# Kernel optimization log

Measured on AMD Instinct MI355X. Metric: run time of the kernel, lower is better.

The kernel has to match this reference:

```python
import jax, jax.numpy as jnp
import numpy as np

B, N, DIM = 1, 32768, 512
H, DH = 8, 64            # heads, dim_head
INNER = H * DH           # 512
L = 64                   # n_cluster = clip(N // (16*16) + 1, 16, 64) = 64 landmarks
ITERS = 6                # pinv_iterations
KS = 33                  # residual_conv_kernel


def setup_inputs() -> dict:
    key = jax.random.key(0)
    k1, k2, k3, k4, k5 = jax.random.split(key, 5)
    x = jax.random.normal(k1, (B, N, DIM), jnp.float32)
    labels = jax.random.randint(k2, (N,), 0, L, jnp.int32)  # kmeans cluster ids (no_grad constants)
    Wqkv = jax.random.normal(k3, (DIM, 3 * INNER), jnp.float32) * 0.02
    Wout = jax.random.normal(k4, (INNER, DIM), jnp.float32) * 0.02
    bout = jnp.zeros((DIM,), jnp.float32)
    res_kernel = jax.random.normal(k5, (H, 1, KS, 1), jnp.float32) * 0.05  # depthwise conv, groups=H
    return dict(x=x, Wqkv=Wqkv, Wout=Wout, bout=bout, res_kernel=res_kernel, labels=labels)


def _pinv(a, iters=ITERS):
    # Moore-Penrose via Newton-Schulz, matching moore_penrose_iter_pinv (global max normalization)
    abs_a = jnp.abs(a)
    z = a.swapaxes(-1, -2) / (abs_a.sum(-1).max() * abs_a.sum(-2).max())
    I = jnp.eye(a.shape[-1], dtype=a.dtype)
    for _ in range(iters):
        az = a @ z
        z = 0.25 * z @ (13.0 * I - az @ (15.0 * I - az @ (7.0 * I - az)))
    return z


def _pool_mean(t, seg):
    # ragged per-cluster mean: t [b,h,n,d], seg [n] sorted cluster ids -> [b,h,L,d]
    b, h, n, d = t.shape
    flat = t.transpose(2, 0, 1, 3).reshape(n, b * h * d)
    sums = jax.ops.segment_sum(flat, seg, num_segments=L)
    counts = jax.ops.segment_sum(jnp.ones((n,), t.dtype), seg, num_segments=L)
    means = sums / jnp.maximum(counts, 1.0)[:, None]
    return means.reshape(L, b, h, d).transpose(1, 2, 0, 3)


def reference(x, Wqkv, Wout, bout, res_kernel, labels):
    # cluster sort / unsort (mirrors x[:, index] ... out[:, index_ori])
    index = jnp.argsort(labels)
    index_ori = jnp.argsort(index)
    seg = labels[index]                      # sorted segment ids
    xp = x[:, index]

    qkv = xp @ Wqkv                          # [b,n,3*inner]
    q, k, v = jnp.split(qkv, 3, axis=-1)
    to_bhnd = lambda t: t.reshape(B, N, H, DH).transpose(0, 2, 1, 3)
    q, k, v = to_bhnd(q), to_bhnd(k), to_bhnd(v)

    ql = _pool_mean(q, seg)                  # [b,h,L,d]
    kl = _pool_mean(k, seg)

    # note: original forward never multiplies by self.scale
    attn1 = jax.nn.softmax(jnp.einsum('bhnd,bhld->bhnl', q, kl), axis=-1)   # [b,h,n,L]
    attn2 = jax.nn.softmax(jnp.einsum('bhid,bhjd->bhij', ql, kl), axis=-1)  # [b,h,L,L]
    attn3 = jax.nn.softmax(jnp.einsum('bhld,bhnd->bhln', ql, k), axis=-1)   # [b,h,L,n]

    out = attn1 @ (_pinv(attn2) @ (attn3 @ v))                              # [b,h,n,d]

    # residual depthwise conv over token axis (Conv2d(h,h,(33,1),groups=h))
    res = jax.lax.conv_general_dilated(
        v, res_kernel, window_strides=(1, 1),
        padding=((KS // 2, KS // 2), (0, 0)),
        dimension_numbers=('NCHW', 'OIHW', 'NCHW'),
        feature_group_count=H)
    out = out + res

    out = out.transpose(0, 2, 1, 3).reshape(B, N, INNER)
    out = out @ Wout + bout
    return out[:, index_ori]
```

## Files before the change

kernel.cpp:

```cpp
#include <hip/hip_runtime.h>
#include <hip/hip_bf16.h>

#define N_TOK 32768
#define DIMC  512
#define NH    8
#define DHD   64
#define NL    64
#define KSZ   33
#define QKVC  1536
#define NCHUNK 64

typedef _Float16 f16;
typedef _Float16 f16x8 __attribute__((ext_vector_type(8)));
typedef _Float16 f16x4 __attribute__((ext_vector_type(4)));
typedef float    f32x4 __attribute__((ext_vector_type(4)));

#define GLOAD_LDS16(gp, lp) \
    __builtin_amdgcn_global_load_lds((const __attribute__((address_space(1))) void*)(gp), \
                                     (__attribute__((address_space(3))) void*)(lp), 16, 0, 0)

__global__ void transpose_k(const float* __restrict__ W, f16* __restrict__ WT, int R, int C) {
    __shared__ float tile[32][33];
    int bx = blockIdx.x * 32, by = blockIdx.y * 32;
    int tx = threadIdx.x, ty = threadIdx.y;
    #pragma unroll
    for (int i = 0; i < 32; i += 8)
        tile[ty + i][tx] = W[(size_t)(by + ty + i) * C + bx + tx];
    __syncthreads();
    #pragma unroll
    for (int i = 0; i < 32; i += 8)
        WT[(size_t)(bx + ty + i) * R + by + tx] = (f16)tile[tx][ty + i];
}

__global__ void hist_k(const int* __restrict__ labels, int* __restrict__ counts) {
    __shared__ int hloc[NL];
    int t = threadIdx.x;
    if (t < NL) hloc[t] = 0;
    __syncthreads();
    int i = blockIdx.x * 256 + t;
    atomicAdd(&hloc[labels[i]], 1);
    __syncthreads();
    if (t < NL) atomicAdd(&counts[t], hloc[t]);
}

__global__ void scan_k(const int* __restrict__ counts, int* __restrict__ base) {
    if (threadIdx.x == 0) {
        int s = 0;
        for (int l = 0; l < NL; ++l) { base[l] = s; s += counts[l]; }
    }
}

__global__ __launch_bounds__(256) void compact_k(const int* __restrict__ labels,
                                                 const int* __restrict__ base,
                                                 int* __restrict__ indexArr) {
    const int l = blockIdx.x;
    __shared__ int wtot[4];
    __shared__ int s_run;
    int t = threadIdx.x, lane = t & 63, w = t >> 6;
    if (t == 0) s_run = base[l];
    __syncthreads();
    for (int c0 = 0; c0 < N_TOK; c0 += 256) {
        int ii = c0 + t;
        bool flag = (labels[ii] == l);
        unsigned long long mask = __ballot(flag);
        int before = __popcll(mask & ((1ull << lane) - 1ull));
        if (lane == 0) wtot[w] = __popcll(mask);
        __syncthreads();
        int off = 0;
        #pragma unroll
        for (int ww = 0; ww < 4; ++ww) off += (ww < w) ? wtot[ww] : 0;
        int tot = wtot[0] + wtot[1] + wtot[2] + wtot[3];
        int rb = s_run;
        if (flag) indexArr[rb + off + before] = ii;
        __syncthreads();
        if (t == 0) s_run = rb + tot;
    }
}

__global__ __launch_bounds__(256) void gather_cvt_k(const float4* __restrict__ x4,
                                                    const int* __restrict__ indexArr,
                                                    f16x4* __restrict__ xh4) {
    int t = threadIdx.x;
    int row = blockIdx.x * 2 + (t >> 7);
    int c4 = t & 127;
    int j = indexArr[row];
    float4 v = x4[(size_t)j * 128 + c4];
    f16x4 o = { (f16)v.x, (f16)v.y, (f16)v.z, (f16)v.w };
    xh4[(size_t)row * 128 + c4] = o;
}

template<int BNTOT, bool OUT_F32, int NY>
__global__ __launch_bounds__(512, 4) void gemm_k512(const f16* __restrict__ A, const f16* __restrict__ BT,
                                                    void* __restrict__ Cout, const float* __restrict__ bias,
                                                    const int* __restrict__ scatterIdx) {
    constexpr int K = 512;
    constexpr int NKT = K / 32;
    __shared__ f16 As[3][128 * 32];
    __shared__ f16 Bs[3][256 * 32];
    const int t = threadIdx.x;
    const int orig = blockIdx.x + gridDim.x * blockIdx.y;
    constexpr int NWG = 256 * NY;
    constexpr int CPX = NWG / 8;
    const int lin = (orig & 7) * CPX + (orig >> 3);
    const int mBase = (lin / NY) * 128;
    const int nBase = (lin % NY) * 256;
    const int w = t >> 6, lane = t & 63;
    const int wm = w >> 2, wn = w & 3;
    const int lr = lane & 15, lk = lane >> 4;
    const int kc = (lk ^ ((lr >> 1) & 3)) * 8;
    f32x4 acc[4][4];
    #pragma unroll
    for (int m = 0; m < 4; ++m)
        #pragma unroll
        for (int n = 0; n < 4; ++n) acc[m][n] = (f32x4){0.f, 0.f, 0.f, 0.f};

    auto stage = [&](int buf, int kt) {
        {
            int id = t;
            int row = id >> 2, c = id & 3;
            int cg = c ^ ((row >> 1) & 3);
            GLOAD_LDS16(&A[(size_t)(mBase + row) * K + kt * 32 + cg * 8],
                        &As[buf][(size_t)(w * 64) * 8]);
        }
        #pragma unroll
        for (int r = 0; r < 2; ++r) {
            int id = r * 512 + t;
            int row = id >> 2, c = id & 3;
            int cg = c ^ ((row >> 1) & 3);
            GLOAD_LDS16(&BT[(size_t)(nBase + row) * K + kt * 32 + cg * 8],
                        &Bs[buf][(size_t)(r * 512 + w * 64) * 8]);
        }
    };
    auto compute = [&](int buf) {
        f16x8 af[4], bf[4];
        #pragma unroll
        for (int m = 0; m < 4; ++m)
            af[m] = *(const f16x8*)&As[buf][(wm * 64 + m * 16 + lr) * 32 + kc];
        #pragma unroll
        for (int n = 0; n < 4; ++n)
            bf[n] = *(const f16x8*)&Bs[buf][(wn * 64 + n * 16 + lr) * 32 + kc];
        #pragma unroll
        for (int m = 0; m < 4; ++m)
            #pragma unroll
            for (int n = 0; n < 4; ++n)
                acc[m][n] = __builtin_amdgcn_mfma_f32_16x16x32_f16(bf[n], af[m], acc[m][n], 0, 0, 0);
    };

    stage(0, 0);
    asm volatile("" ::: "memory");
    stage(1, 1);
    for (int kt = 0; kt < NKT; ++kt) {
        if (kt < NKT - 1) {
            asm volatile("s_waitcnt vmcnt(3)" ::: "memory");
        } else {
            asm volatile("s_waitcnt vmcnt(0)" ::: "memory");
        }
        __builtin_amdgcn_s_barrier();
        if (kt + 2 < NKT) stage((kt + 2) % 3, kt + 2);
        compute(kt % 3);
    }

    #pragma unroll
    for (int m = 0; m < 4; ++m) {
        int row = mBase + wm * 64 + m * 16 + lr;
        int srow = OUT_F32 ? scatterIdx[row] : row;
        #pragma unroll
        for (int n = 0; n < 4; ++n) {
            int col = nBase + wn * 64 + n * 16 + lk * 4;
            if constexpr (OUT_F32) {
                float4 bv = *(const float4*)&bias[col];
                float4 sv = make_float4(acc[m][n][0] + bv.x, acc[m][n][1] + bv.y,
                                        acc[m][n][2] + bv.z, acc[m][n][3] + bv.w);
                *(float4*)&((float*)Cout)[(size_t)srow * BNTOT + col] = sv;
            } else {
                f16x4 hv = { (f16)acc[m][n][0], (f16)acc[m][n][1],
                             (f16)acc[m][n][2], (f16)acc[m][n][3] };
                *(f16x4*)&((f16*)Cout)[(size_t)srow * BNTOT + col] = hv;
            }
        }
    }
}

__global__ __launch_bounds__(256) void pool_part_k(const f16* __restrict__ qkvh,
                                                   const int* __restrict__ base,
                                                   const int* __restrict__ counts,
                                                   float* __restrict__ psum) {
    int l = blockIdx.x, g = blockIdx.y;
    int t = threadIdx.x;
    int c = t & 127, rg = t >> 7;
    int b0 = base[l], cnt = counts[l];
    f32x4 a0 = {0.f,0.f,0.f,0.f}, a1 = {0.f,0.f,0.f,0.f};
    for (int p = g * 2 + rg; p < cnt; p += 8) {
        f16x8 v = *(const f16x8*)&qkvh[(size_t)(b0 + p) * QKVC + c * 8];
        a0[0] += (float)v[0]; a0[1] += (float)v[1]; a0[2] += (float)v[2]; a0[3] += (float)v[3];
        a1[0] += (float)v[4]; a1[1] += (float)v[5]; a1[2] += (float)v[6]; a1[3] += (float)v[7];
    }
    __shared__ f32x4 red[2][128][2];
    red[rg][c][0] = a0; red[rg][c][1] = a1;
    __syncthreads();
    if (t < 128) {
        f32x4 s0 = red[0][t][0] + red[1][t][0];
        f32x4 s1 = red[0][t][1] + red[1][t][1];
        size_t o = ((size_t)g * NL + l) * 1024 + t * 8;
        *(f32x4*)&psum[o] = s0;
        *(f32x4*)&psum[o + 4] = s1;
    }
}

__global__ __launch_bounds__(256) void pool_fin_k(const float* __restrict__ psum,
                                                  const int* __restrict__ counts,
                                                  float* __restrict__ ql, float* __restrict__ kl,
                                                  f16* __restrict__ qlh, f16* __restrict__ klh) {
    int l = blockIdx.x;
    int t = threadIdx.x;
    int bse = t * 4;
    float inv = 1.0f / (float)(counts[l] > 0 ? counts[l] : 1);
    f32x4 s = {0.f,0.f,0.f,0.f};
    #pragma unroll
    for (int g = 0; g < 4; ++g)
        s += *(const f32x4*)&psum[((size_t)g * NL + l) * 1024 + bse];
    s *= inv;
    f16x4 hv = { (f16)s[0], (f16)s[1], (f16)s[2], (f16)s[3] };
    if (bse < 512) {
        int h = bse >> 6, d0 = bse & 63;
        size_t o = ((size_t)(h * 64 + l)) * 64 + d0;
        *(f32x4*)&ql[o] = s;
        *(f16x4*)&qlh[o] = hv;
    } else {
        int bb = bse - 512;
        int h = bb >> 6, d0 = bb & 63;
        size_t o = ((size_t)(h * 64 + l)) * 64 + d0;
        *(f32x4*)&kl[o] = s;
        *(f16x4*)&klh[o] = hv;
    }
}

__global__ __launch_bounds__(256) void attn2_k(const float* __restrict__ ql, const float* __restrict__ kl,
                                               float* __restrict__ a_out, float* __restrict__ mrow,
                                               float* __restrict__ mcol) {
    int h = blockIdx.x;
    __shared__ float qs[64][65], ks[64][65], a[64][65];
    __shared__ float red[64][4];
    __shared__ float rowv[64], colv[64];
    int t = threadIdx.x;
    for (int idx = t; idx < 4096; idx += 256) {
        int r = idx >> 6, c = idx & 63;
        qs[r][c] = ql[h * 4096 + idx];
        ks[r][c] = kl[h * 4096 + idx];
    }
    __syncthreads();
    int i = t >> 2, q4 = t & 3, j0 = q4 * 16;
    float o[16];
    #pragma unroll
    for (int jj = 0; jj < 16; ++jj) o[jj] = 0.f;
    for (int d = 0; d < 64; ++d) {
        float qv = qs[i][d];
        #pragma unroll
        for (int jj = 0; jj < 16; ++jj) o[jj] += qv * ks[j0 + jj][d];
    }
    float pmx = o[0];
    #pragma unroll
    for (int jj = 1; jj < 16; ++jj) pmx = fmaxf(pmx, o[jj]);
    red[i][q4] = pmx;
    __syncthreads();
    float rm = fmaxf(fmaxf(red[i][0], red[i][1]), fmaxf(red[i][2], red[i][3]));
    float psum = 0.f;
    #pragma unroll
    for (int jj = 0; jj < 16; ++jj) { o[jj] = expf(o[jj] - rm); psum += o[jj]; }
    __syncthreads();
    red[i][q4] = psum;
    __syncthreads();
    float rs = red[i][0] + red[i][1] + red[i][2] + red[i][3];
    float inv = 1.0f / rs;
    #pragma unroll
    for (int jj = 0; jj < 16; ++jj) { o[jj] *= inv; a[i][j0 + jj] = o[jj]; }
    __syncthreads();
    for (int idx = t; idx < 4096; idx += 256) a_out[h * 4096 + idx] = a[idx >> 6][idx & 63];
    float rsum = 0.f;
    #pragma unroll
    for (int jj = 0; jj < 16; ++jj) rsum += o[jj];
    __syncthreads();
    red[i][q4] = rsum;
    __syncthreads();
    if (q4 == 0) rowv[i] = red[i][0] + red[i][1] + red[i][2] + red[i][3];
    float csum = 0.f;
    #pragma unroll
    for (int jj = 0; jj < 16; ++jj) csum += a[j0 + jj][i];
    __syncthreads();
    red[i][q4] = csum;
    __syncthreads();
    if (q4 == 0) colv[i] = red[i][0] + red[i][1] + red[i][2] + red[i][3];
    __syncthreads();
    if (t == 0) {
        float mr = rowv[0], mc = colv[0];
        for (int j = 1; j < 64; ++j) { mr = fmaxf(mr, rowv[j]); mc = fmaxf(mc, colv[j]); }
        mrow[h] = mr; mcol[h] = mc;
    }
}

__global__ __launch_bounds__(256) void pinv_zmatT_k(const float* __restrict__ a_g,
                                                    const float* __restrict__ mrow,
                                                    const float* __restrict__ mcol,
                                                    const float* __restrict__ T,
                                                    f16* __restrict__ MthHi, f16* __restrict__ MthLo) {
    const int h = blockIdx.x;
    __shared__ float zf[64][68];
    __shared__ float Cf[64][68];
    __shared__ f16 aRh[64][72], aRl[64][72];
    __shared__ f16 zFh[64][72], zFl[64][72];
    __shared__ f16 cRh[64][72], cRl[64][72];
    __shared__ f16 ceCh[64][72], ceCl[64][72];
    __shared__ f16 dCh[64][72], dCl[64][72];
    const int t = threadIdx.x;
    const int w = t >> 6, lane = t & 63;
    const int lr = lane & 15, lk = lane >> 4;
    float mr = mrow[0], mc = mcol[0];
    #pragma unroll
    for (int k = 1; k < 8; ++k) { mr = fmaxf(mr, mrow[k]); mc = fmaxf(mc, mcol[k]); }
    const float inv0 = 1.0f / (mr * mc);
    for (int idx = t; idx < 4096; idx += 256) {
        int r = idx >> 6, c = idx & 63;
        float av = a_g[h * 4096 + idx];
        f16 hv = (f16)av;
        aRh[r][c] = hv; aRl[r][c] = (f16)(av - (float)hv);
        zf[c][r] = av * inv0;
    }
    __syncthreads();

    f32x4 po[4];
    auto product = [&](const f16 (*Xh)[72], const f16 (*Xl)[72],
                       const f16 (*Yh)[72], const f16 (*Yl)[72]) {
        #pragma unroll
        for (int n = 0; n < 4; ++n) po[n] = (f32x4){0.f, 0.f, 0.f, 0.f};
        #pragma unroll
        for (int ck = 0; ck < 2; ++ck) {
            f16x8 axh = *(const f16x8*)&Xh[w * 16 + lr][ck * 32 + lk * 8];
            f16x8 axl = *(const f16x8*)&Xl[w * 16 + lr][ck * 32 + lk * 8];
            #pragma unroll
            for (int n = 0; n < 4; ++n) {
                f16x8 byh = *(const f16x8*)&Yh[n * 16 + lr][ck * 32 + lk * 8];
                f16x8 byl = *(const f16x8*)&Yl[n * 16 + lr][ck * 32 + lk * 8];
                po[n] = __builtin_amdgcn_mfma_f32_16x16x32_f16(byh, axh, po[n], 0, 0, 0);
                po[n] = __builtin_amdgcn_mfma_f32_16x16x32_f16(byl, axh, po[n], 0, 0, 0);
                po[n] = __builtin_amdgcn_mfma_f32_16x16x32_f16(byh, axl, po[n], 0, 0, 0);
            }
        }
    };

    for (int it = 0; it < 6; ++it) {
        for (int idx = t; idx < 4096; idx += 256) {
            int r = idx >> 6, c = idx & 63;
            float v = zf[r][c]; f16 hv = (f16)v;
            zFh[c][r] = hv; zFl[c][r] = (f16)(v - (float)hv);
        }
        __syncthreads();
        product(aRh, aRl, zFh, zFl);
        #pragma unroll
        for (int n = 0; n < 4; ++n) {
            int r = w * 16 + lr, c0 = n * 16 + lk * 4;
            *(float4*)&Cf[r][c0] = make_float4(po[n][0], po[n][1], po[n][2], po[n][3]);
            #pragma unroll
            for (int j = 0; j < 4; ++j) {
                float v = po[n][j]; f16 hv = (f16)v; f16 lv = (f16)(v - (float)hv);
                cRh[r][c0 + j] = hv; cRl[r][c0 + j] = lv;
                ceCh[c0 + j][r] = hv; ceCl[c0 + j][r] = lv;
            }
        }
        __syncthreads();
        product(cRh, cRl, ceCh, ceCl);
        #pragma unroll
        for (int n = 0; n < 4; ++n)
            #pragma unroll
            for (int j = 0; j < 4; ++j) {
                int r = w * 16 + lr, c = n * 16 + lk * 4 + j;
                float v = 7.f * Cf[r][c] - po[n][j];
                f16 hv = (f16)v;
                dCh[c][r] = hv; dCl[c][r] = (f16)(v - (float)hv);
            }
        __syncthreads();
        product(cRh, cRl, dCh, dCl);
        #pragma unroll
        for (int n = 0; n < 4; ++n)
            #pragma unroll
            for (int j = 0; j < 4; ++j) {
                int r = w * 16 + lr, c = n * 16 + lk * 4 + j;
                float v = 15.f * Cf[r][c] - po[n][j];
                f16 hv = (f16)v;
                ceCh[c][r] = hv; ceCl[c][r] = (f16)(v - (float)hv);
            }
        __syncthreads();
        for (int idx = t; idx < 4096; idx += 256) {
            int r = idx >> 6, c = idx & 63;
            float v = zf[r][c]; f16 hv = (f16)v;
            zFh[r][c] = hv; zFl[r][c] = (f16)(v - (float)hv);
        }
        __syncthreads();
        product(zFh, zFl, ceCh, ceCl);
        #pragma unroll
        for (int n = 0; n < 4; ++n)
            #pragma unroll
            for (int j = 0; j < 4; ++j) {
                int r = w * 16 + lr, c = n * 16 + lk * 4 + j;
                zf[r][c] = 0.25f * (13.f * zf[r][c] - po[n][j]);
            }
        __syncthreads();
    }
    for (int idx = t; idx < 4096; idx += 256) {
        int r = idx >> 6, c = idx & 63;
        float v = zf[r][c]; f16 hv = (f16)v;
        zFh[r][c] = hv; zFl[r][c] = (f16)(v - (float)hv);
        float tv = T[h * 4096 + idx]; f16 th = (f16)tv;
        dCh[c][r] = th; dCl[c][r] = (f16)(tv - (float)th);
    }
    __syncthreads();
    product(zFh, zFl, dCh, dCl);
    #pragma unroll
    for (int n = 0; n < 4; ++n)
        #pragma unroll
        for (int j = 0; j < 4; ++j) {
            int r = w * 16 + lr, c = n * 16 + lk * 4 + j;
            float v = po[n][j]; f16 hv = (f16)v;
            MthHi[h * 4096 + c * 64 + r] = hv;
            MthLo[h * 4096 + c * 64 + r] = (f16)(v - (float)hv);
        }
}

__global__ __launch_bounds__(256) void attn3_k(const f16* __restrict__ qkvh, const f16* __restrict__ qlh,
                                               float* __restrict__ pm, float* __restrict__ ps,
                                               float* __restrict__ pacc) {
    const int cx = blockIdx.x, h = blockIdx.y;
    const int t = threadIdx.x;
    const int w = t >> 6, lane = t & 63;
    const int lr = lane & 15, hi = lane >> 4;
    __shared__ f16 Qls[64 * 64];
    __shared__ f16 Ks[64 * 64];
    __shared__ f16 vT[64 * 72];
    __shared__ f16 Ps[64 * 72];
    __shared__ float fsh[64];

    #pragma unroll
    for (int pss = 0; pss < 2; ++pss) {
        int q = pss * 256 + t;
        int r = q >> 3, cs = (q & 7) ^ (r & 7);
        GLOAD_LDS16(&qlh[(size_t)h * 4096 + r * 64 + cs * 8], &Qls[(size_t)(pss * 256 + w * 64) * 8]);
    }
    float m_reg = -1e30f, s_reg = 0.f;
    f32x4 accT[4];
    #pragma unroll
    for (int lf = 0; lf < 4; ++lf) accT[lf] = (f32x4){0.f, 0.f, 0.f, 0.f};

    const int vk8 = t & 7, vnn = t >> 3;

    for (int sub = 0; sub < 8; ++sub) {
        const int n0 = cx * 512 + sub * 64;
        __syncthreads();
        #pragma unroll
        for (int pss = 0; pss < 2; ++pss) {
            int q = pss * 256 + t;
            int r = q >> 3, cs = (q & 7) ^ (r & 7);
            GLOAD_LDS16(&qkvh[(size_t)(n0 + r) * QKVC + 512 + h * 64 + cs * 8],
                        &Ks[(size_t)(pss * 256 + w * 64) * 8]);
        }
        #pragma unroll
        for (int p2 = 0; p2 < 2; ++p2) {
            int n = vnn + 32 * p2;
            f16x8 rv = *(const f16x8*)&qkvh[(size_t)(n0 + n) * QKVC + 1024 + h * 64 + vk8 * 8];
            #pragma unroll
            for (int i = 0; i < 8; ++i) {
                int e = i ^ vk8;
                vT[(vk8 * 8 + e) * 72 + n] = rv[e];
            }
        }
        __syncthreads();
        f32x4 c[4];
        #pragma unroll
        for (int kf = 0; kf < 4; ++kf) c[kf] = (f32x4){0.f, 0.f, 0.f, 0.f};
        const int lq = w * 16 + lr;
        #pragma unroll
        for (int ks = 0; ks < 2; ++ks) {
            f16x8 bf = *(const f16x8*)&Qls[lq * 64 + (((ks * 4 + hi) ^ (lq & 7)) * 8)];
            #pragma unroll
            for (int kf = 0; kf < 4; ++kf) {
                int rn = kf * 16 + lr;
                f16x8 af = *(const f16x8*)&Ks[rn * 64 + (((ks * 4 + hi) ^ (rn & 7)) * 8)];
                c[kf] = __builtin_amdgcn_mfma_f32_16x16x32_f16(af, bf, c[kf], 0, 0, 0);
            }
        }
        float tmax = -1e30f;
        #pragma unroll
        for (int kf = 0; kf < 4; ++kf)
            #pragma unroll
            for (int j = 0; j < 4; ++j) tmax = fmaxf(tmax, c[kf][j]);
        tmax = fmaxf(tmax, __shfl_xor(tmax, 16));
        tmax = fmaxf(tmax, __shfl_xor(tmax, 32));
        float newm = fmaxf(m_reg, tmax);
        float fct = __expf(m_reg - newm);
        float psum = 0.f;
        #pragma unroll
        for (int kf = 0; kf < 4; ++kf) {
            f16x4 pk;
            #pragma unroll
            for (int j = 0; j < 4; ++j) {
                float e = __expf(c[kf][j] - newm);
                psum += e;
                pk[j] = (f16)e;
            }
            *(f16x4*)&Ps[lq * 72 + kf * 16 + hi * 4] = pk;
        }
        psum += __shfl_xor(psum, 16);
        psum += __shfl_xor(psum, 32);
        s_reg = s_reg * fct + psum;
        m_reg = newm;
        if (hi == 0) fsh[lq] = fct;
        __syncthreads();
        #pragma unroll
        for (int lf = 0; lf < 4; ++lf) {
            f32x4 fr = *(const f32x4*)&fsh[lf * 16 + hi * 4];
            accT[lf] *= fr;
        }
        #pragma unroll
        for (int ks = 0; ks < 2; ++ks) {
            f16x8 bf = *(const f16x8*)&vT[(w * 16 + lr) * 72 + ks * 32 + hi * 8];
            #pragma unroll
            for (int lf = 0; lf < 4; ++lf) {
                f16x8 af = *(const f16x8*)&Ps[(lf * 16 + lr) * 72 + ks * 32 + hi * 8];
                accT[lf] = __builtin_amdgcn_mfma_f32_16x16x32_f16(af, bf, accT[lf], 0, 0, 0);
            }
        }
    }
    int part = h * NCHUNK + cx;
    if (hi == 0) {
        pm[part * 64 + w * 16 + lr] = m_reg;
        ps[part * 64 + w * 16 + lr] = s_reg;
    }
    #pragma unroll
    for (int lf = 0; lf < 4; ++lf)
        #pragma unroll
        for (int j = 0; j < 4; ++j)
            pacc[((size_t)part * 64 + (lf * 16 + hi * 4 + j)) * 64 + (w * 16 + lr)] = accT[lf][j];
}

__global__ void attn3_merge_k(const float* __restrict__ pm, const float* __restrict__ ps,
                              const float* __restrict__ pacc, float* __restrict__ T) {
    int l = blockIdx.x, h = blockIdx.y, d = threadIdx.x;
    float m = -1e30f;
    for (int c = 0; c < NCHUNK; ++c) m = fmaxf(m, pm[(h * NCHUNK + c) * 64 + l]);
    float s = 0.f, a = 0.f;
    for (int c = 0; c < NCHUNK; ++c) {
        float wgt = __expf(pm[(h * NCHUNK + c) * 64 + l] - m);
        s += ps[(h * NCHUNK + c) * 64 + l] * wgt;
        a += pacc[((size_t)(h * NCHUNK + c) * 64 + l) * 64 + d] * wgt;
    }
    T[(h * 64 + l) * 64 + d] = a / s;
}

__global__ __launch_bounds__(256) void attn1_k(const f16* __restrict__ qkvh, const f16* __restrict__ klh,
                                               const f16* __restrict__ MthHi, const f16* __restrict__ MthLo,
                                               const float* __restrict__ resk, f16* __restrict__ Yh) {
    const int h = blockIdx.y;
    const int p0 = blockIdx.x * 128;
    const int t = threadIdx.x;
    const int w = t >> 6, lane = t & 63;
    const int lr = lane & 15, hi = lane >> 4;
    __shared__ f16 QPs[128][72];
    __shared__ f16 Ks[64][72];
    __shared__ f16 Mhi[64][72];
    __shared__ f16 Mlo[64][72];
    __shared__ f16 vt[160][72];

    #pragma unroll
    for (int i = 0; i < 4; ++i) {
        int id = i * 256 + t, row = id >> 3, c8 = id & 7;
        *(f16x8*)&QPs[row][c8 * 8] = *(const f16x8*)&qkvh[(size_t)(p0 + row) * QKVC + h * 64 + c8 * 8];
    }
    #pragma unroll
    for (int i = 0; i < 2; ++i) {
        int id = i * 256 + t, row = id >> 3, c8 = id & 7;
        *(f16x8*)&Ks[row][c8 * 8]  = *(const f16x8*)&klh[h * 4096 + id * 8];
        *(f16x8*)&Mhi[row][c8 * 8] = *(const f16x8*)&MthHi[h * 4096 + id * 8];
        *(f16x8*)&Mlo[row][c8 * 8] = *(const f16x8*)&MthLo[h * 4096 + id * 8];
    }
    for (int id = t; id < 160 * 8; id += 256) {
        int rr = id >> 3, c8 = id & 7;
        int pg = p0 - 16 + rr;
        int4 v = {0, 0, 0, 0};
        if (pg >= 0 && pg < N_TOK)
            v = *(const int4*)&qkvh[(size_t)pg * QKVC + 1024 + h * 64 + c8 * 8];
        *(int4*)&vt[rr][c8 * 8] = v;
    }
    float wk[KSZ];
    #pragma unroll
    for (int k = 0; k < KSZ; ++k) wk[k] = resk[h * KSZ + k];
    __syncthreads();

    f32x4 c[4][2];
    #pragma unroll
    for (int lf = 0; lf < 4; ++lf)
        #pragma unroll
        for (int nf = 0; nf < 2; ++nf) c[lf][nf] = (f32x4){0.f, 0.f, 0.f, 0.f};
    #pragma unroll
    for (int ks = 0; ks < 2; ++ks) {
        f16x8 af[4], bf[2];
        #pragma unroll
        for (int lf = 0; lf < 4; ++lf) af[lf] = *(const f16x8*)&Ks[lf * 16 + lr][ks * 32 + hi * 8];
        #pragma unroll
        for (int nf = 0; nf < 2; ++nf) bf[nf] = *(const f16x8*)&QPs[w * 32 + nf * 16 + lr][ks * 32 + hi * 8];
        #pragma unroll
        for (int lf = 0; lf < 4; ++lf)
            #pragma unroll
            for (int nf = 0; nf < 2; ++nf)
                c[lf][nf] = __builtin_amdgcn_mfma_f32_16x16x32_f16(af[lf], bf[nf], c[lf][nf], 0, 0, 0);
    }

    #pragma unroll
    for (int nf = 0; nf < 2; ++nf) {
        float m = -1e30f;
        #pragma unroll
        for (int lf = 0; lf < 4; ++lf)
            #pragma unroll
            for (int j = 0; j < 4; ++j) m = fmaxf(m, c[lf][nf][j]);
        m = fmaxf(m, __shfl_xor(m, 16));
        m = fmaxf(m, __shfl_xor(m, 32));
        float s = 0.f;
        #pragma unroll
        for (int lf = 0; lf < 4; ++lf)
            #pragma unroll
            for (int j = 0; j < 4; ++j) { float e = __expf(c[lf][nf][j] - m); c[lf][nf][j] = e; s += e; }
        s += __shfl_xor(s, 16);
        s += __shfl_xor(s, 32);
        float inv = 1.0f / s;
        #pragma unroll
        for (int lf = 0; lf < 4; ++lf) {
            f16x4 pk;
            #pragma unroll
            for (int j = 0; j < 4; ++j) pk[j] = (f16)(c[lf][nf][j] * inv);
            *(f16x4*)&QPs[w * 32 + nf * 16 + lr][lf * 16 + hi * 4] = pk;
        }
    }

    f32x4 o[2][4];
    #pragma unroll
    for (int nf = 0; nf < 2; ++nf)
        #pragma unroll
        for (int df = 0; df < 4; ++df) o[nf][df] = (f32x4){0.f, 0.f, 0.f, 0.f};
    #pragma unroll
    for (int ks = 0; ks < 2; ++ks) {
        f16x8 pa[2], bh[4], bl[4];
        #pragma unroll
        for (int nf = 0; nf < 2; ++nf) pa[nf] = *(const f16x8*)&QPs[w * 32 + nf * 16 + lr][ks * 32 + hi * 8];
        #pragma unroll
        for (int df = 0; df < 4; ++df) {
            bh[df] = *(const f16x8*)&Mhi[df * 16 + lr][ks * 32 + hi * 8];
            bl[df] = *(const f16x8*)&Mlo[df * 16 + lr][ks * 32 + hi * 8];
        }
        #pragma unroll
        for (int nf = 0; nf < 2; ++nf)
            #pragma unroll
            for (int df = 0; df < 4; ++df) {
                o[nf][df] = __builtin_amdgcn_mfma_f32_16x16x32_f16(pa[nf], bh[df], o[nf][df], 0, 0, 0);
                o[nf][df] = __builtin_amdgcn_mfma_f32_16x16x32_f16(pa[nf], bl[df], o[nf][df], 0, 0, 0);
            }
    }

    #pragma unroll
    for (int nf = 0; nf < 2; ++nf)
        #pragma unroll
        for (int df = 0; df < 4; ++df)
            #pragma unroll
            for (int j = 0; j < 4; ++j)
                QPs[w * 32 + nf * 16 + hi * 4 + j][df * 16 + lr] = (f16)(o[nf][df][j]);
    __syncthreads();

    const int d = t & 63, rg = t >> 6;
    #pragma unroll
    for (int hh = 0; hh < 2; ++hh) {
        const int r0 = rg * 32 + hh * 16;
        float col[48];
        #pragma unroll
        for (int j = 0; j < 48; ++j) col[j] = (float)vt[r0 + j][d];
        #pragma unroll
        for (int pp = 0; pp < 16; ++pp) {
            float acc = 0.f;
            #pragma unroll
            for (int k = 0; k < KSZ; ++k) acc += wk[k] * col[pp + k];
            int row = r0 + pp;
            Yh[(size_t)(p0 + row) * 512 + h * 64 + d] = (f16)(acc + (float)QPs[row][d]);
        }
    }
}

extern "C" void kernel_launch(void* const* d_in, const int* in_sizes, int n_in,
                              void* d_out, int out_size, void* d_ws, size_t ws_size,
                              hipStream_t stream) {
    const float* x    = (const float*)d_in[0];
    const float* Wqkv = (const float*)d_in[1];
    const float* Wout = (const float*)d_in[2];
    const float* bout = (const float*)d_in[3];
    const float* resk = (const float*)d_in[4];
    const int*   labels = (const int*)d_in[5];
    float* out = (float*)d_out;

    char* w = (char*)d_ws;
    size_t off = 0;
    auto alloc = [&](size_t bytes) {
        void* p = w + off;
        off += (bytes + 255) & ~(size_t)255;
        return p;
    };
    f16* xh     = (f16*)alloc((size_t)N_TOK * DIMC * 2);
    f16* qkvh   = (f16*)alloc((size_t)N_TOK * QKVC * 2);
    f16* WqkvT  = (f16*)alloc((size_t)QKVC * DIMC * 2);
    f16* WoutT  = (f16*)alloc((size_t)DIMC * DIMC * 2);
    f16* Yh     = (f16*)alloc((size_t)N_TOK * DIMC * 2);
    int* counts = (int*)alloc(NL * 4);
    int* baseA  = (int*)alloc(NL * 4);
    int* indexA = (int*)alloc((size_t)N_TOK * 4);
    float* ql   = (float*)alloc((size_t)NH * 64 * 64 * 4);
    float* kl   = (float*)alloc((size_t)NH * 64 * 64 * 4);
    f16* qlh    = (f16*)alloc((size_t)NH * 64 * 64 * 2);
    f16* klh    = (f16*)alloc((size_t)NH * 64 * 64 * 2);
    float* a2   = (float*)alloc((size_t)NH * 64 * 64 * 4);
    float* mrow = (float*)alloc(NH * 4);
    float* mcol = (float*)alloc(NH * 4);
    float* Tb   = (float*)alloc((size_t)NH * 64 * 64 * 4);
    f16* MthHi  = (f16*)alloc((size_t)NH * 64 * 64 * 2);
    f16* MthLo  = (f16*)alloc((size_t)NH * 64 * 64 * 2);
    float* pm   = (float*)alloc((size_t)NH * NCHUNK * 64 * 4);
    float* ps   = (float*)alloc((size_t)NH * NCHUNK * 64 * 4);
    float* pacc = (float*)alloc((size_t)NH * NCHUNK * 64 * 64 * 4);
    float* psum = (float*)alloc((size_t)4 * NL * 1024 * 4);

    hipMemsetAsync(counts, 0, NL * 4, stream);

    hist_k<<<N_TOK / 256, 256, 0, stream>>>(labels, counts);
    scan_k<<<1, 64, 0, stream>>>(counts, baseA);
    compact_k<<<NL, 256, 0, stream>>>(labels, baseA, indexA);
    gather_cvt_k<<<N_TOK / 2, 256, 0, stream>>>((const float4*)x, indexA, (f16x4*)xh);
    transpose_k<<<dim3(QKVC / 32, DIMC / 32), dim3(32, 8), 0, stream>>>(Wqkv, WqkvT, DIMC, QKVC);
    transpose_k<<<dim3(DIMC / 32, DIMC / 32), dim3(32, 8), 0, stream>>>(Wout, WoutT, DIMC, DIMC);
    gemm_k512<QKVC, false, 6><<<dim3(N_TOK / 128, QKVC / 256), 512, 0, stream>>>(xh, WqkvT, qkvh, nullptr, nullptr);
    pool_part_k<<<dim3(NL, 4), 256, 0, stream>>>(qkvh, baseA, counts, psum);
    pool_fin_k<<<NL, 256, 0, stream>>>(psum, counts, ql, kl, qlh, klh);
    attn2_k<<<NH, 256, 0, stream>>>(ql, kl, a2, mrow, mcol);
    attn3_k<<<dim3(NCHUNK, NH), 256, 0, stream>>>(qkvh, qlh, pm, ps, pacc);
    attn3_merge_k<<<dim3(NL, NH), 64, 0, stream>>>(pm, ps, pacc, Tb);
    pinv_zmatT_k<<<NH, 256, 0, stream>>>(a2, mrow, mcol, Tb, MthHi, MthLo);
    attn1_k<<<dim3(N_TOK / 128, NH), 256, 0, stream>>>(qkvh, klh, MthHi, MthLo, resk, Yh);
    gemm_k512<DIMC, true, 2><<<dim3(N_TOK / 128, DIMC / 256), 512, 0, stream>>>(Yh, WoutT, out, bout, indexA);
}
```

Baseline: 338.9 us.

## Overlap pinv Newton-Schulz iterations with attn3 blocks; fold scan into consumers

```diff
diff --git a/kernel.cpp b/kernel.cpp
--- a/kernel.cpp
+++ b/kernel.cpp
@@ -43,21 +43,18 @@
     if (t < NL) atomicAdd(&counts[t], hloc[t]);
 }
 
-__global__ void scan_k(const int* __restrict__ counts, int* __restrict__ base) {
-    if (threadIdx.x == 0) {
-        int s = 0;
-        for (int l = 0; l < NL; ++l) { base[l] = s; s += counts[l]; }
-    }
-}
-
 __global__ __launch_bounds__(256) void compact_k(const int* __restrict__ labels,
-                                                 const int* __restrict__ base,
+                                                 const int* __restrict__ counts,
                                                  int* __restrict__ indexArr) {
     const int l = blockIdx.x;
     __shared__ int wtot[4];
     __shared__ int s_run;
     int t = threadIdx.x, lane = t & 63, w = t >> 6;
-    if (t == 0) s_run = base[l];
+    if (t == 0) {
+        int s = 0;
+        for (int j = 0; j < l; ++j) s += counts[j];
+        s_run = s;
+    }
     __syncthreads();
     for (int c0 = 0; c0 < N_TOK; c0 += 256) {
         int ii = c0 + t;
@@ -182,13 +179,14 @@
 }
 
 __global__ __launch_bounds__(256) void pool_part_k(const f16* __restrict__ qkvh,
-                                                   const int* __restrict__ base,
                                                    const int* __restrict__ counts,
                                                    float* __restrict__ psum) {
     int l = blockIdx.x, g = blockIdx.y;
     int t = threadIdx.x;
     int c = t & 127, rg = t >> 7;
-    int b0 = base[l], cnt = counts[l];
+    int b0 = 0;
+    for (int j = 0; j < l; ++j) b0 += counts[j];
+    int cnt = counts[l];
     f32x4 a0 = {0.f,0.f,0.f,0.f}, a1 = {0.f,0.f,0.f,0.f};
     for (int p = g * 2 + rg; p < cnt; p += 8) {
         f16x8 v = *(const f16x8*)&qkvh[(size_t)(b0 + p) * QKVC + c * 8];
@@ -298,145 +296,134 @@
     }
 }
 
-__global__ __launch_bounds__(256) void pinv_zmatT_k(const float* __restrict__ a_g,
+__global__ __launch_bounds__(256) void attn3_pinv_k(const f16* __restrict__ qkvh,
+                                                    const f16* __restrict__ qlh,
+                                                    float* __restrict__ pm, float* __restrict__ ps,
+                                                    float* __restrict__ pacc,
+                                                    const float* __restrict__ a_g,
                                                     const float* __restrict__ mrow,
                                                     const float* __restrict__ mcol,
-                                                    const float* __restrict__ T,
-                                                    f16* __restrict__ MthHi, f16* __restrict__ MthLo) {
-    const int h = blockIdx.x;
-    __shared__ float zf[64][68];
-    __shared__ float Cf[64][68];
-    __shared__ f16 aRh[64][72], aRl[64][72];
-    __shared__ f16 zFh[64][72], zFl[64][72];
-    __shared__ f16 cRh[64][72], cRl[64][72];
-    __shared__ f16 ceCh[64][72], ceCl[64][72];
-    __shared__ f16 dCh[64][72], dCl[64][72];
+                                                    float* __restrict__ zg) {
+    union ShU {
+        struct { f16 Qls[64 * 64]; f16 Ks[64 * 64]; f16 vT[64 * 72]; f16 Ps[64 * 72]; float fsh[64]; } a3;
+        struct { f16 zRh[64][72], zRl[64][72], cRh[64][72], cRl[64][72],
+                 Xh[64][72], Xl[64][72], Yh[64][72], Yl[64][72]; } pv;
+    };
+    __shared__ ShU sh;
     const int t = threadIdx.x;
     const int w = t >> 6, lane = t & 63;
-    const int lr = lane & 15, lk = lane >> 4;
-    float mr = mrow[0], mc = mcol[0];
-    #pragma unroll
-    for (int k = 1; k < 8; ++k) { mr = fmaxf(mr, mrow[k]); mc = fmaxf(mc, mcol[k]); }
-    const float inv0 = 1.0f / (mr * mc);
-    for (int idx = t; idx < 4096; idx += 256) {
-        int r = idx >> 6, c = idx & 63;
-        float av = a_g[h * 4096 + idx];
-        f16 hv = (f16)av;
-        aRh[r][c] = hv; aRl[r][c] = (f16)(av - (float)hv);
-        zf[c][r] = av * inv0;
-    }
-    __syncthreads();
-
-    f32x4 po[4];
-    auto product = [&](const f16 (*Xh)[72], const f16 (*Xl)[72],
-                       const f16 (*Yh)[72], const f16 (*Yl)[72]) {
-        #pragma unroll
-        for (int n = 0; n < 4; ++n) po[n] = (f32x4){0.f, 0.f, 0.f, 0.f};
-        #pragma unroll
-        for (int ck = 0; ck < 2; ++ck) {
-            f16x8 axh = *(const f16x8*)&Xh[w * 16 + lr][ck * 32 + lk * 8];
-            f16x8 axl = *(const f16x8*)&Xl[w * 16 + lr][ck * 32 + lk * 8];
-            #pragma unroll
-            for (int n = 0; n < 4; ++n) {
-                f16x8 byh = *(const f16x8*)&Yh[n * 16 + lr][ck * 32 + lk * 8];
-                f16x8 byl = *(const f16x8*)&Yl[n * 16 + lr][ck * 32 + lk * 8];
-                po[n] = __builtin_amdgcn_mfma_f32_16x16x32_f16(byh, axh, po[n], 0, 0, 0);
-                po[n] = __builtin_amdgcn_mfma_f32_16x16x32_f16(byl, axh, po[n], 0, 0, 0);
-                po[n] = __builtin_amdgcn_mfma_f32_16x16x32_f16(byh, axl, po[n], 0, 0, 0);
-            }
-        }
-    };
-
-    for (int it = 0; it < 6; ++it) {
+    const int lr = lane & 15;
+    const int h = blockIdx.y;
+
+    if (blockIdx.x == 0) {
+        const int lk = lane >> 4;
+        f16 (&zRh)[64][72] = sh.pv.zRh; f16 (&zRl)[64][72] = sh.pv.zRl;
+        f16 (&cRh)[64][72] = sh.pv.cRh; f16 (&cRl)[64][72] = sh.pv.cRl;
+        f16 (&Xh)[64][72]  = sh.pv.Xh;  f16 (&Xl)[64][72]  = sh.pv.Xl;
+        f16 (&Yh)[64][72]  = sh.pv.Yh;  f16 (&Yl)[64][72]  = sh.pv.Yl;
+        float mr = mrow[0], mc = mcol[0];
+        #pragma unroll
+        for (int k = 1; k < 8; ++k) { mr = fmaxf(mr, mrow[k]); mc = fmaxf(mc, mcol[k]); }
+        const float inv0 = 1.0f / (mr * mc);
         for (int idx = t; idx < 4096; idx += 256) {
             int r = idx >> 6, c = idx & 63;
-            float v = zf[r][c]; f16 hv = (f16)v;
-            zFh[c][r] = hv; zFl[c][r] = (f16)(v - (float)hv);
+            float zv = a_g[h * 4096 + idx] * inv0;
+            f16 hv = (f16)zv;
+            zRh[c][r] = hv; zRl[c][r] = (f16)(zv - (float)hv);
         }
         __syncthreads();
-        product(aRh, aRl, zFh, zFl);
-        #pragma unroll
-        for (int n = 0; n < 4; ++n) {
-            int r = w * 16 + lr, c0 = n * 16 + lk * 4;
-            *(float4*)&Cf[r][c0] = make_float4(po[n][0], po[n][1], po[n][2], po[n][3]);
-            #pragma unroll
-            for (int j = 0; j < 4; ++j) {
-                float v = po[n][j]; f16 hv = (f16)v; f16 lv = (f16)(v - (float)hv);
-                cRh[r][c0 + j] = hv; cRl[r][c0 + j] = lv;
-                ceCh[c0 + j][r] = hv; ceCl[c0 + j][r] = lv;
+
+        f32x4 po[4];
+        auto product = [&](const f16 (*Lh)[72], const f16 (*Ll)[72],
+                           const f16 (*Rh)[72], const f16 (*Rl)[72]) {
+            #pragma unroll
+            for (int n = 0; n < 4; ++n) po[n] = (f32x4){0.f, 0.f, 0.f, 0.f};
+            #pragma unroll
+            for (int ck = 0; ck < 2; ++ck) {
+                f16x8 axh = *(const f16x8*)&Lh[w * 16 + lr][ck * 32 + lk * 8];
+                f16x8 axl = *(const f16x8*)&Ll[w * 16 + lr][ck * 32 + lk * 8];
+                #pragma unroll
+                for (int n = 0; n < 4; ++n) {
+                    f16x8 byh = *(const f16x8*)&Rh[n * 16 + lr][ck * 32 + lk * 8];
+                    f16x8 byl = *(const f16x8*)&Rl[n * 16 + lr][ck * 32 + lk * 8];
+                    po[n] = __builtin_amdgcn_mfma_f32_16x16x32_f16(byh, axh, po[n], 0, 0, 0);
+                    po[n] = __builtin_amdgcn_mfma_f32_16x16x32_f16(byl, axh, po[n], 0, 0, 0);
+                    po[n] = __builtin_amdgcn_mfma_f32_16x16x32_f16(byh, axl, po[n], 0, 0, 0);
+                }
             }
-        }
-        __syncthreads();
-        product(cRh, cRl, ceCh, ceCl);
-        #pragma unroll
-        for (int n = 0; n < 4; ++n)
-            #pragma unroll
-            for (int j = 0; j < 4; ++j) {
-                int r = w * 16 + lr, c = n * 16 + lk * 4 + j;
-                float v = 7.f * Cf[r][c] - po[n][j];
-                f16 hv = (f16)v;
-                dCh[c][r] = hv; dCl[c][r] = (f16)(v - (float)hv);
+        };
+
+        for (int it = 0; it < 6; ++it) {
+            for (int idx = t; idx < 4096; idx += 256) {
+                int r = idx >> 6, c = idx & 63;
+                float av = a_g[h * 4096 + idx];
+                f16 ah = (f16)av;
+                Xh[r][c] = ah; Xl[r][c] = (f16)(av - (float)ah);
+                float zv = (float)zRh[r][c] + (float)zRl[r][c];
+                f16 zh = (f16)zv;
+                Yh[c][r] = zh; Yl[c][r] = (f16)(zv - (float)zh);
             }
-        __syncthreads();
-        product(cRh, cRl, dCh, dCl);
-        #pragma unroll
-        for (int n = 0; n < 4; ++n)
-            #pragma unroll
-            for (int j = 0; j < 4; ++j) {
-                int r = w * 16 + lr, c = n * 16 + lk * 4 + j;
-                float v = 15.f * Cf[r][c] - po[n][j];
-                f16 hv = (f16)v;
-                ceCh[c][r] = hv; ceCl[c][r] = (f16)(v - (float)hv);
-            }
-        __syncthreads();
+            __syncthreads();
+            product(Xh, Xl, Yh, Yl);
+            __syncthreads();
+            #pragma unroll
+            for (int n = 0; n < 4; ++n)
+                #pragma unroll
+                for (int j = 0; j < 4; ++j) {
+                    int r = w * 16 + lr, c = n * 16 + lk * 4 + j;
+                    float v = po[n][j]; f16 hv = (f16)v; f16 lv = (f16)(v - (float)hv);
+                    cRh[r][c] = hv; cRl[r][c] = lv;
+                    Xh[c][r] = hv;  Xl[c][r] = lv;
+                }
+            __syncthreads();
+            product(cRh, cRl, Xh, Xl);
+            #pragma unroll
+            for (int n = 0; n < 4; ++n)
+                #pragma unroll
+                for (int j = 0; j < 4; ++j) {
+                    int r = w * 16 + lr, c = n * 16 + lk * 4 + j;
+                    float v = 7.f * ((float)cRh[r][c] + (float)cRl[r][c]) - po[n][j];
+                    f16 hv = (f16)v;
+                    Yh[c][r] = hv; Yl[c][r] = (f16)(v - (float)hv);
+                }
+            __syncthreads();
+            product(cRh, cRl, Yh, Yl);
+            #pragma unroll
+            for (int n = 0; n < 4; ++n)
+                #pragma unroll
+                for (int j = 0; j < 4; ++j) {
+                    int r = w * 16 + lr, c = n * 16 + lk * 4 + j;
+                    float v = 15.f * ((float)cRh[r][c] + (float)cRl[r][c]) - po[n][j];
+                    f16 hv = (f16)v;
+                    Xh[c][r] = hv; Xl[c][r] = (f16)(v - (float)hv);
+                }
+            __syncthreads();
+            product(zRh, zRl, Xh, Xl);
+            #pragma unroll
+            for (int n = 0; n < 4; ++n)
+                #pragma unroll
+                for (int j = 0; j < 4; ++j) {
+                    int r = w * 16 + lr, c = n * 16 + lk * 4 + j;
+                    float v = 0.25f * (13.f * ((float)zRh[r][c] + (float)zRl[r][c]) - po[n][j]);
+                    f16 hv = (f16)v;
+                    zRh[r][c] = hv; zRl[r][c] = (f16)(v - (float)hv);
+                }
+            __syncthreads();
+        }
         for (int idx = t; idx < 4096; idx += 256) {
             int r = idx >> 6, c = idx & 63;
-            float v = zf[r][c]; f16 hv = (f16)v;
-            zFh[r][c] = hv; zFl[r][c] = (f16)(v - (float)hv);
-        }
-        __syncthreads();
-        product(zFh, zFl, ceCh, ceCl);
-        #pragma unroll
-        for (int n = 0; n < 4; ++n)
-            #pragma unroll
-            for (int j = 0; j < 4; ++j) {
-                int r = w * 16 + lr, c = n * 16 + lk * 4 + j;
-                zf[r][c] = 0.25f * (13.f * zf[r][c] - po[n][j]);
-            }
-        __syncthreads();
-    }
-    for (int idx = t; idx < 4096; idx += 256) {
-        int r = idx >> 6, c = idx & 63;
-        float v = zf[r][c]; f16 hv = (f16)v;
-        zFh[r][c] = hv; zFl[r][c] = (f16)(v - (float)hv);
-        float tv = T[h * 4096 + idx]; f16 th = (f16)tv;
-        dCh[c][r] = th; dCl[c][r] = (f16)(tv - (float)th);
-    }
-    __syncthreads();
-    product(zFh, zFl, dCh, dCl);
-    #pragma unroll
-    for (int n = 0; n < 4; ++n)
-        #pragma unroll
-        for (int j = 0; j < 4; ++j) {
-            int r = w * 16 + lr, c = n * 16 + lk * 4 + j;
-            float v = po[n][j]; f16 hv = (f16)v;
-            MthHi[h * 4096 + c * 64 + r] = hv;
-            MthLo[h * 4096 + c * 64 + r] = (f16)(v - (float)hv);
-        }
-}
-
-__global__ __launch_bounds__(256) void attn3_k(const f16* __restrict__ qkvh, const f16* __restrict__ qlh,
-                                               float* __restrict__ pm, float* __restrict__ ps,
-                                               float* __restrict__ pacc) {
-    const int cx = blockIdx.x, h = blockIdx.y;
-    const int t = threadIdx.x;
-    const int w = t >> 6, lane = t & 63;
-    const int lr = lane & 15, hi = lane >> 4;
-    __shared__ f16 Qls[64 * 64];
-    __shared__ f16 Ks[64 * 64];
-    __shared__ f16 vT[64 * 72];
-    __shared__ f16 Ps[64 * 72];
-    __shared__ float fsh[64];
+            zg[h * 4096 + idx] = (float)zRh[r][c] + (float)zRl[r][c];
+        }
+        return;
+    }
+
+    const int cx = blockIdx.x - 1;
+    const int hi = lane >> 4;
+    f16* Qls = sh.a3.Qls;
+    f16* Ks  = sh.a3.Ks;
+    f16* vT  = sh.a3.vT;
+    f16* Ps  = sh.a3.Ps;
+    float* fsh = sh.a3.fsh;
 
     #pragma unroll
     for (int pss = 0; pss < 2; ++pss) {
@@ -552,6 +539,49 @@
         a += pacc[((size_t)(h * NCHUNK + c) * 64 + l) * 64 + d] * wgt;
     }
     T[(h * 64 + l) * 64 + d] = a / s;
+}
+
+__global__ __launch_bounds__(256) void zmatT_fin_k(const float* __restrict__ zg,
+                                                   const float* __restrict__ T,
+                                                   f16* __restrict__ MthHi, f16* __restrict__ MthLo) {
+    const int h = blockIdx.x;
+    __shared__ f16 zFh[64][72], zFl[64][72], tCh[64][72], tCl[64][72];
+    const int t = threadIdx.x;
+    const int w = t >> 6, lane = t & 63;
+    const int lr = lane & 15, lk = lane >> 4;
+    for (int idx = t; idx < 4096; idx += 256) {
+        int r = idx >> 6, c = idx & 63;
+        float zv = zg[h * 4096 + idx]; f16 zh = (f16)zv;
+        zFh[r][c] = zh; zFl[r][c] = (f16)(zv - (float)zh);
+        float tv = T[h * 4096 + idx]; f16 th = (f16)tv;
+        tCh[c][r] = th; tCl[c][r] = (f16)(tv - (float)th);
+    }
+    __syncthreads();
+    f32x4 po[4];
+    #pragma unroll
+    for (int n = 0; n < 4; ++n) po[n] = (f32x4){0.f, 0.f, 0.f, 0.f};
+    #pragma unroll
+    for (int ck = 0; ck < 2; ++ck) {
+        f16x8 axh = *(const f16x8*)&zFh[w * 16 + lr][ck * 32 + lk * 8];
+        f16x8 axl = *(const f16x8*)&zFl[w * 16 + lr][ck * 32 + lk * 8];
+        #pragma unroll
+        for (int n = 0; n < 4; ++n) {
+            f16x8 byh = *(const f16x8*)&tCh[n * 16 + lr][ck * 32 + lk * 8];
+            f16x8 byl = *(const f16x8*)&tCl[n * 16 + lr][ck * 32 + lk * 8];
+            po[n] = __builtin_amdgcn_mfma_f32_16x16x32_f16(byh, axh, po[n], 0, 0, 0);
+            po[n] = __builtin_amdgcn_mfma_f32_16x16x32_f16(byl, axh, po[n], 0, 0, 0);
+            po[n] = __builtin_amdgcn_mfma_f32_16x16x32_f16(byh, axl, po[n], 0, 0, 0);
+        }
+    }
+    #pragma unroll
+    for (int n = 0; n < 4; ++n)
+        #pragma unroll
+        for (int j = 0; j < 4; ++j) {
+            int r = w * 16 + lr, c = n * 16 + lk * 4 + j;
+            float v = po[n][j]; f16 hv = (f16)v;
+            MthHi[h * 4096 + c * 64 + r] = hv;
+            MthLo[h * 4096 + c * 64 + r] = (f16)(v - (float)hv);
+        }
 }
 
 __global__ __launch_bounds__(256) void attn1_k(const f16* __restrict__ qkvh, const f16* __restrict__ klh,
@@ -713,7 +743,6 @@
     f16* WoutT  = (f16*)alloc((size_t)DIMC * DIMC * 2);
     f16* Yh     = (f16*)alloc((size_t)N_TOK * DIMC * 2);
     int* counts = (int*)alloc(NL * 4);
-    int* baseA  = (int*)alloc(NL * 4);
     int* indexA = (int*)alloc((size_t)N_TOK * 4);
     float* ql   = (float*)alloc((size_t)NH * 64 * 64 * 4);
     float* kl   = (float*)alloc((size_t)NH * 64 * 64 * 4);
@@ -723,6 +752,7 @@
     float* mrow = (float*)alloc(NH * 4);
     float* mcol = (float*)alloc(NH * 4);
     float* Tb   = (float*)alloc((size_t)NH * 64 * 64 * 4);
+    float* zg   = (float*)alloc((size_t)NH * 64 * 64 * 4);
     f16* MthHi  = (f16*)alloc((size_t)NH * 64 * 64 * 2);
     f16* MthLo  = (f16*)alloc((size_t)NH * 64 * 64 * 2);
     float* pm   = (float*)alloc((size_t)NH * NCHUNK * 64 * 4);
@@ -733,18 +763,17 @@
     hipMemsetAsync(counts, 0, NL * 4, stream);
 
     hist_k<<<N_TOK / 256, 256, 0, stream>>>(labels, counts);
-    scan_k<<<1, 64, 0, stream>>>(counts, baseA);
-    compact_k<<<NL, 256, 0, stream>>>(labels, baseA, indexA);
+    compact_k<<<NL, 256, 0, stream>>>(labels, counts, indexA);
     gather_cvt_k<<<N_TOK / 2, 256, 0, stream>>>((const float4*)x, indexA, (f16x4*)xh);
     transpose_k<<<dim3(QKVC / 32, DIMC / 32), dim3(32, 8), 0, stream>>>(Wqkv, WqkvT, DIMC, QKVC);
     transpose_k<<<dim3(DIMC / 32, DIMC / 32), dim3(32, 8), 0, stream>>>(Wout, WoutT, DIMC, DIMC);
     gemm_k512<QKVC, false, 6><<<dim3(N_TOK / 128, QKVC / 256), 512, 0, stream>>>(xh, WqkvT, qkvh, nullptr, nullptr);
-    pool_part_k<<<dim3(NL, 4), 256, 0, stream>>>(qkvh, baseA, counts, psum);
+    pool_part_k<<<dim3(NL, 4), 256, 0, stream>>>(qkvh, counts, psum);
     pool_fin_k<<<NL, 256, 0, stream>>>(psum, counts, ql, kl, qlh, klh);
     attn2_k<<<NH, 256, 0, stream>>>(ql, kl, a2, mrow, mcol);
-    attn3_k<<<dim3(NCHUNK, NH), 256, 0, stream>>>(qkvh, qlh, pm, ps, pacc);
+    attn3_pinv_k<<<dim3(NCHUNK + 1, NH), 256, 0, stream>>>(qkvh, qlh, pm, ps, pacc, a2, mrow, mcol, zg);
     attn3_merge_k<<<dim3(NL, NH), 64, 0, stream>>>(pm, ps, pacc, Tb);
-    pinv_zmatT_k<<<NH, 256, 0, stream>>>(a2, mrow, mcol, Tb, MthHi, MthLo);
+    zmatT_fin_k<<<NH, 256, 0, stream>>>(zg, Tb, MthHi, MthLo);
     attn1_k<<<dim3(N_TOK / 128, NH), 256, 0, stream>>>(qkvh, klh, MthHi, MthLo, resk, Yh);
     gemm_k512<DIMC, true, 2><<<dim3(N_TOK / 128, DIMC / 256), 512, 0, stream>>>(Yh, WoutT, out, bout, indexA);
 }
```

Measured after the change: 338.3 us. No clear change (-0.2%).
